# Performance work log

Hardware: AMD Instinct MI355X
Metric: run time of the kernel (lower is better)

The kernel has to match this reference:

```python
import jax, jax.numpy as jnp
import numpy as np

N_NODES = 50000
N_EDGES = 600000
F_IN = 128
DIM_H = 256
N_CLASSES = 40
BN_EPS = 1e-5


def setup_inputs() -> dict:
    key = jax.random.key(0)
    ks = jax.random.split(key, 10)
    x = jax.random.normal(ks[0], (N_NODES, F_IN), dtype=jnp.float32)
    edge_index = jax.random.randint(ks[1], (2, N_EDGES), 0, N_NODES, dtype=jnp.int64)
    s1 = 1.0 / np.sqrt(F_IN)
    s2 = 1.0 / np.sqrt(DIM_H)
    W1 = jax.random.uniform(ks[2], (F_IN, DIM_H), jnp.float32, -s1, s1)
    b1 = jax.random.uniform(ks[3], (DIM_H,), jnp.float32, -s1, s1)
    gamma = jnp.ones((DIM_H,), jnp.float32)
    beta = jnp.zeros((DIM_H,), jnp.float32)
    W2 = jax.random.uniform(ks[4], (DIM_H, DIM_H), jnp.float32, -s2, s2)
    b2 = jax.random.uniform(ks[5], (DIM_H,), jnp.float32, -s2, s2)
    Wlin = jax.random.uniform(ks[6], (DIM_H, N_CLASSES), jnp.float32, -s2, s2)
    blin = jax.random.uniform(ks[7], (N_CLASSES,), jnp.float32, -s2, s2)
    return {"x": x, "edge_index": edge_index, "W1": W1, "b1": b1,
            "gamma": gamma, "beta": beta, "W2": W2, "b2": b2,
            "Wlin": Wlin, "blin": blin}


def reference(x, edge_index, W1, b1, gamma, beta, W2, b2, Wlin, blin):
    src, dst = edge_index[0], edge_index[1]
    # GIN sum aggregation: agg[i] = sum_{(j->i)} x[j]; eps = 0 (default)
    agg = jax.ops.segment_sum(x[src], dst, num_segments=N_NODES)  # [N, F_IN]
    h = x + agg
    # MLP: Linear -> BatchNorm1d (training-mode batch stats) -> ReLU -> Linear -> ReLU
    h = h @ W1 + b1                               # [N, DIM_H]
    mean = jnp.mean(h, axis=0)
    var = jnp.var(h, axis=0)                      # biased, as torch BN uses for normalization
    h = (h - mean) * jax.lax.rsqrt(var + BN_EPS) * gamma + beta
    h = jax.nn.relu(h)
    h = jax.nn.relu(h @ W2 + b2)                  # MLP final ReLU; outer x.relu() is idempotent
    return h @ Wlin + blin                        # [N, N_CLASSES]
```

## Files before the change

kernel.cpp:

```cpp
#include <hip/hip_runtime.h>

#define F_IN 128
#define DIM_H 256
#define N_CLASSES 40
#define BN_EPS 1e-5f
#define M_PAD 50176

typedef short bf16x8 __attribute__((ext_vector_type(8)));
typedef float f32x4 __attribute__((ext_vector_type(4)));

__device__ __forceinline__ unsigned short f2bf(float f) {
    union { float f; unsigned u; } v; v.f = f;
    unsigned r = v.u + 0x7fff + ((v.u >> 16) & 1);
    return (unsigned short)(r >> 16);
}
__device__ __forceinline__ float bf2f(unsigned short u) {
    union { unsigned u; float f; } v; v.u = ((unsigned)u) << 16;
    return v.f;
}
__device__ __forceinline__ float4 bf2f4(ushort4 u) {
    return make_float4(bf2f(u.x), bf2f(u.y), bf2f(u.z), bf2f(u.w));
}

__global__ void hist_kernel(const int* __restrict__ dst, int* __restrict__ hist, int nE) {
    int e = blockIdx.x * blockDim.x + threadIdx.x;
    if (e >= nE) return;
    atomicAdd(&hist[dst[e]], 1);
}

__global__ void scan_blocks_kernel(const int* __restrict__ hist,
                                   int* __restrict__ blockSums, int M) {
    __shared__ int lds[256];
    int t = threadIdx.x;
    int i = blockIdx.x * 256 + t;
    lds[t] = (i < M) ? hist[i] : 0;
    __syncthreads();
    for (int off = 128; off > 0; off >>= 1) {
        if (t < off) lds[t] += lds[t + off];
        __syncthreads();
    }
    if (t == 0) blockSums[blockIdx.x] = lds[0];
}

__global__ void scan_offsets_kernel(const int* __restrict__ blockSums,
                                    int* __restrict__ blockOffs,
                                    int nB, int* __restrict__ start, int M, int nE) {
    __shared__ int lds[256];
    int t = threadIdx.x;
    int orig = (t < nB) ? blockSums[t] : 0;
    lds[t] = orig;
    __syncthreads();
    for (int off = 1; off < 256; off <<= 1) {
        int v = (t >= off) ? lds[t - off] : 0;
        __syncthreads();
        lds[t] += v;
        __syncthreads();
    }
    if (t < nB) blockOffs[t] = lds[t] - orig;
    if (t == 0) start[M] = nE;
}

__global__ void scan_final_kernel(const int* __restrict__ hist,
                                  const int* __restrict__ blockOffs,
                                  int* __restrict__ start, int M) {
    __shared__ int lds[256];
    int t = threadIdx.x;
    int i = blockIdx.x * 256 + t;
    int orig = (i < M) ? hist[i] : 0;
    lds[t] = orig;
    __syncthreads();
    for (int off = 1; off < 256; off <<= 1) {
        int v = (t >= off) ? lds[t - off] : 0;
        __syncthreads();
        lds[t] += v;
        __syncthreads();
    }
    if (i < M) start[i] = blockOffs[blockIdx.x] + lds[t] - orig;
}

__global__ void fill_kernel(const int* __restrict__ src, const int* __restrict__ dst,
                            const int* __restrict__ start, int* __restrict__ cursor,
                            int* __restrict__ order, int nE) {
    int e = blockIdx.x * blockDim.x + threadIdx.x;
    if (e >= nE) return;
    int d = dst[e];
    int pos = start[d] + atomicAdd(&cursor[d], 1);
    order[pos] = src[e];
}

__global__ void prep_kernel(const float* __restrict__ x, unsigned short* __restrict__ xb,
                            const float* __restrict__ W1, const float* __restrict__ W2,
                            const float* __restrict__ Wl,
                            unsigned short* __restrict__ W1t,
                            unsigned short* __restrict__ W2t,
                            unsigned short* __restrict__ Wlt,
                            unsigned short* __restrict__ A1pad,
                            unsigned short* __restrict__ h1pad,
                            int XQ) {
    int idx = blockIdx.x * 256 + threadIdx.x;
    if (idx < XQ) {
        float4 v = ((const float4*)x)[idx];
        ushort4 o;
        o.x = f2bf(v.x); o.y = f2bf(v.y); o.z = f2bf(v.z); o.w = f2bf(v.w);
        ((ushort4*)xb)[idx] = o;
        return;
    }
    int j = idx - XQ;
    if (j < 32768) {
        int n = j >> 7, k = j & 127;
        W1t[j] = f2bf(W1[k * DIM_H + n]);
    } else if (j < 32768 + 65536) {
        int i = j - 32768;
        int n = i >> 8, k = i & 255;
        W2t[i] = f2bf(W2[k * DIM_H + n]);
    } else if (j < 32768 + 65536 + 16384) {
        int i = j - 98304;
        int n = i >> 8, k = i & 255;
        Wlt[i] = f2bf((n < N_CLASSES) ? Wl[k * N_CLASSES + n] : 0.f);
    } else if (j < 114688 + 4608) {
        int i = j - 114688;
        if (i < 1536) ((ushort4*)A1pad)[i] = make_ushort4(0, 0, 0, 0);
        else ((ushort4*)h1pad)[i - 1536] = make_ushort4(0, 0, 0, 0);
    }
}

__global__ void gather_agg_kernel(const float* __restrict__ x,
                                  const unsigned short* __restrict__ xb,
                                  const int* __restrict__ order,
                                  const int* __restrict__ start,
                                  unsigned short* __restrict__ A1, int M) {
    int node = blockIdx.x * 8 + (threadIdx.x >> 5);
    if (node >= M) return;
    int lane = threadIdx.x & 31;
    const ushort4* xv = (const ushort4*)xb;
    float4 a0 = ((const float4*)x)[(size_t)node * 32 + lane];
    float4 a1 = make_float4(0.f, 0.f, 0.f, 0.f);
    float4 a2 = a1, a3 = a1;
    int e0 = start[node], e1 = start[node + 1];
    int e = e0;
    for (; e + 4 <= e1; e += 4) {
        int s0 = order[e], s1 = order[e + 1], s2 = order[e + 2], s3 = order[e + 3];
        float4 v0 = bf2f4(xv[(size_t)s0 * 32 + lane]);
        float4 v1 = bf2f4(xv[(size_t)s1 * 32 + lane]);
        float4 v2 = bf2f4(xv[(size_t)s2 * 32 + lane]);
        float4 v3 = bf2f4(xv[(size_t)s3 * 32 + lane]);
        a0.x += v0.x; a0.y += v0.y; a0.z += v0.z; a0.w += v0.w;
        a1.x += v1.x; a1.y += v1.y; a1.z += v1.z; a1.w += v1.w;
        a2.x += v2.x; a2.y += v2.y; a2.z += v2.z; a2.w += v2.w;
        a3.x += v3.x; a3.y += v3.y; a3.z += v3.z; a3.w += v3.w;
    }
    for (; e < e1; ++e) {
        float4 v = bf2f4(xv[(size_t)order[e] * 32 + lane]);
        a1.x += v.x; a1.y += v.y; a1.z += v.z; a1.w += v.w;
    }
    float4 t;
    t.x = (a0.x + a1.x) + (a2.x + a3.x);
    t.y = (a0.y + a1.y) + (a2.y + a3.y);
    t.z = (a0.z + a1.z) + (a2.z + a3.z);
    t.w = (a0.w + a1.w) + (a2.w + a3.w);
    ushort4 o;
    o.x = f2bf(t.x); o.y = f2bf(t.y); o.z = f2bf(t.z); o.w = f2bf(t.w);
    ((ushort4*)A1)[(size_t)node * 32 + lane] = o;
}

__global__ void bn_reduce_kernel(const float* __restrict__ partials, int R,
                                 const float* __restrict__ gamma,
                                 const float* __restrict__ beta,
                                 float* __restrict__ scale,
                                 float* __restrict__ shift, int M) {
    __shared__ float ls[256], lss[256];
    int c = blockIdx.x, t = threadIdx.x;
    float s = 0.f, ss = 0.f;
    for (int r = t; r < R; r += 256) {
        s += partials[(long)r * 512 + c];
        ss += partials[(long)r * 512 + 256 + c];
    }
    ls[t] = s; lss[t] = ss;
    __syncthreads();
    for (int o = 128; o > 0; o >>= 1) {
        if (t < o) { ls[t] += ls[t + o]; lss[t] += lss[t + o]; }
        __syncthreads();
    }
    if (t == 0) {
        float inv = 1.0f / (float)M;
        float mean = ls[0] * inv;
        float var = lss[0] * inv - mean * mean;
        float sc = gamma[c] * rsqrtf(var + BN_EPS);
        scale[c] = sc;
        shift[c] = beta[c] - mean * sc;
    }
}

template <int WM, int WN, int K, int MODE>
__global__ __launch_bounds__(WM* WN * 64) void mfma_gemm(
    const unsigned short* __restrict__ A,
    const unsigned short* __restrict__ Bt,
    const float* __restrict__ bias,
    void* __restrict__ Cout,
    const float* __restrict__ scale,
    const float* __restrict__ shift,
    float* __restrict__ partials,
    const unsigned short* __restrict__ Wlt2,
    const float* __restrict__ bias2,
    int M) {
    constexpr int NT = WM * WN * 64;
    constexpr int BM = WM * 64, BN = WN * 64;
    constexpr int S = K / 32;
    constexpr int PITCH = 40;
    constexpr int ACH = BM * 4 / NT;
    constexpr int BCH = BN * 4 / NT;
    constexpr int STAGE = 2 * (BM + BN) * PITCH;
    constexpr int H2PITCH = 264;
    constexpr int H2T = (MODE == 1) ? BM * H2PITCH : 0;
    constexpr int LDSN = STAGE > H2T ? STAGE : H2T;

    __shared__ __align__(16) unsigned short lds[LDSN];
    unsigned short* AsBase = lds;
    unsigned short* BsBase = lds + 2 * BM * PITCH;

    int tid = threadIdx.x;
    int wave = tid >> 6, lane = tid & 63;
    int wm = wave / WN, wn = wave % WN;
    int l15 = lane & 15, q = lane >> 4;
    long row0 = (long)blockIdx.y * BM;
    long col0 = (long)blockIdx.x * BN;

    bf16x8 ar[ACH], br[BCH];

    auto loadAB = [&](int s) {
#pragma unroll
        for (int i = 0; i < ACH; ++i) {
            int ch = tid + i * NT;
            int m = ch >> 2, c = ch & 3;
            ar[i] = *(const bf16x8*)(A + (row0 + m) * K + s * 32 + c * 8);
        }
#pragma unroll
        for (int i = 0; i < BCH; ++i) {
            int ch = tid + i * NT;
            int m = ch >> 2, c = ch & 3;
            br[i] = *(const bf16x8*)(Bt + (col0 + m) * K + s * 32 + c * 8);
        }
    };

    auto writeAB = [&](int buf, int s) {
#pragma unroll
        for (int i = 0; i < ACH; ++i) {
            int ch = tid + i * NT;
            int m = ch >> 2, c = ch & 3;
            bf16x8 v = ar[i];
            if (MODE == 1) {
                int kb = s * 32 + c * 8;
                float4 sc0 = *(const float4*)(scale + kb);
                float4 sc1 = *(const float4*)(scale + kb + 4);
                float4 sh0 = *(const float4*)(shift + kb);
                float4 sh1 = *(const float4*)(shift + kb + 4);
                float scv[8] = {sc0.x, sc0.y, sc0.z, sc0.w, sc1.x, sc1.y, sc1.z, sc1.w};
                float shv[8] = {sh0.x, sh0.y, sh0.z, sh0.w, sh1.x, sh1.y, sh1.z, sh1.w};
#pragma unroll
                for (int j = 0; j < 8; ++j) {
                    float f = bf2f((unsigned short)v[j]);
                    f = fmaxf(f * scv[j] + shv[j], 0.f);
                    v[j] = (short)f2bf(f);
                }
            }
            *(bf16x8*)(&AsBase[buf * BM * PITCH + m * PITCH + c * 8]) = v;
        }
#pragma unroll
        for (int i = 0; i < BCH; ++i) {
            int ch = tid + i * NT;
            int m = ch >> 2, c = ch & 3;
            *(bf16x8*)(&BsBase[buf * BN * PITCH + m * PITCH + c * 8]) = br[i];
        }
    };

    f32x4 acc[4][4] = {};

    loadAB(0);
    writeAB(0, 0);
#pragma unroll
    for (int s = 0; s < S; ++s) {
        if (s + 1 < S) loadAB(s + 1);
        __syncthreads();
        int buf = s & 1;
        bf16x8 af[4], bfr[4];
#pragma unroll
        for (int mt = 0; mt < 4; ++mt)
            af[mt] = *(const bf16x8*)(&AsBase[buf * BM * PITCH + (wm * 64 + mt * 16 + l15) * PITCH + q * 8]);
#pragma unroll
        for (int nt = 0; nt < 4; ++nt)
            bfr[nt] = *(const bf16x8*)(&BsBase[buf * BN * PITCH + (wn * 64 + nt * 16 + l15) * PITCH + q * 8]);
#pragma unroll
        for (int mt = 0; mt < 4; ++mt)
#pragma unroll
            for (int nt = 0; nt < 4; ++nt)
                acc[mt][nt] = __builtin_amdgcn_mfma_f32_16x16x32_bf16(
                    af[mt], bfr[nt], acc[mt][nt], 0, 0, 0);
        if (s + 1 < S) writeAB((s + 1) & 1, s + 1);
    }

    if (MODE == 0) {
#pragma unroll
        for (int nt = 0; nt < 4; ++nt) {
            long col = col0 + wn * 64 + nt * 16 + l15;
            float b = bias[col];
            float s = 0.f, ss = 0.f;
#pragma unroll
            for (int mt = 0; mt < 4; ++mt) {
#pragma unroll
                for (int r = 0; r < 4; ++r) {
                    long row = row0 + wm * 64 + mt * 16 + q * 4 + r;
                    float v = acc[mt][nt][r] + b;
                    if (row < M) {
                        ((unsigned short*)Cout)[row * DIM_H + col] = f2bf(v);
                        s += v; ss += v * v;
                    }
                }
            }
            s += __shfl_xor(s, 16, 64);  s += __shfl_xor(s, 32, 64);
            ss += __shfl_xor(ss, 16, 64); ss += __shfl_xor(ss, 32, 64);
            if (lane < 16) {
                long pr = (long)blockIdx.y * WM + wm;
                partials[pr * 512 + col] = s;
                partials[pr * 512 + 256 + col] = ss;
            }
        }
    } else {
        __syncthreads();
        unsigned short* h2t = lds;
#pragma unroll
        for (int nt = 0; nt < 4; ++nt) {
            int colL = wn * 64 + nt * 16 + l15;
            float b = bias[colL];
#pragma unroll
            for (int mt = 0; mt < 4; ++mt)
#pragma unroll
                for (int r = 0; r < 4; ++r) {
                    int rowL = mt * 16 + q * 4 + r;
                    h2t[rowL * H2PITCH + colL] = f2bf(fmaxf(acc[mt][nt][r] + b, 0.f));
                }
        }
        __syncthreads();
        f32x4 acc3[3] = {};
#pragma unroll
        for (int s = 0; s < 8; ++s) {
            bf16x8 a3 = *(const bf16x8*)(&h2t[(wave * 16 + l15) * H2PITCH + s * 32 + q * 8]);
#pragma unroll
            for (int nt = 0; nt < 3; ++nt) {
                bf16x8 b3 = *(const bf16x8*)(Wlt2 + (nt * 16 + l15) * 256 + s * 32 + q * 8);
                acc3[nt] = __builtin_amdgcn_mfma_f32_16x16x32_bf16(a3, b3, acc3[nt], 0, 0, 0);
            }
        }
#pragma unroll
        for (int nt = 0; nt < 3; ++nt) {
            int col = nt * 16 + l15;
            if (col < N_CLASSES) {
                float b = bias2[col];
#pragma unroll
                for (int r = 0; r < 4; ++r) {
                    long row = row0 + wave * 16 + q * 4 + r;
                    if (row < M) ((float*)Cout)[row * N_CLASSES + col] = acc3[nt][r] + b;
                }
            }
        }
    }
}

extern "C" void kernel_launch(void* const* d_in, const int* in_sizes, int n_in,
                              void* d_out, int out_size, void* d_ws, size_t ws_size,
                              hipStream_t stream) {
    const float* x     = (const float*)d_in[0];
    const int*   ei    = (const int*)d_in[1];
    const float* W1    = (const float*)d_in[2];
    const float* b1    = (const float*)d_in[3];
    const float* gamma = (const float*)d_in[4];
    const float* beta  = (const float*)d_in[5];
    const float* W2    = (const float*)d_in[6];
    const float* b2    = (const float*)d_in[7];
    const float* Wlin  = (const float*)d_in[8];
    const float* blin  = (const float*)d_in[9];
    float* out = (float*)d_out;

    int M  = in_sizes[0] / F_IN;
    int nE = in_sizes[1] / 2;
    const int* srcIdx = ei;
    const int* dstIdx = ei + nE;
    int nB = (M + 255) / 256;
    int gy = (M + 63) / 64;
    int Rpart = gy;
    int XQ = M * 32;

    unsigned short* A1bf  = (unsigned short*)d_ws;
    unsigned short* h1bf  = A1bf + (size_t)M_PAD * F_IN;
    unsigned short* xb    = h1bf + (size_t)M_PAD * DIM_H;
    unsigned short* W1t   = xb + (size_t)M_PAD * F_IN;
    unsigned short* W2t   = W1t + DIM_H * F_IN;
    unsigned short* Wlt   = W2t + DIM_H * DIM_H;
    float*          partials = (float*)(Wlt + 64 * DIM_H);
    float*          scale = partials + (size_t)800 * 512;
    float*          shift = scale + DIM_H;
    int*            hist  = (int*)(shift + DIM_H);
    int*            cursor= hist + M;
    int*            start = cursor + M;
    int*            blockSums = start + (M + 1);
    int*            blockOffs = blockSums + 256;
    int*            order = blockOffs + 256;

    hipMemsetAsync(hist, 0, (size_t)2 * M * sizeof(int), stream);

    int tB = 256;
    hist_kernel<<<(nE + tB - 1) / tB, tB, 0, stream>>>(dstIdx, hist, nE);
    scan_blocks_kernel<<<nB, 256, 0, stream>>>(hist, blockSums, M);
    scan_offsets_kernel<<<1, 256, 0, stream>>>(blockSums, blockOffs, nB, start, M, nE);
    scan_final_kernel<<<nB, 256, 0, stream>>>(hist, blockOffs, start, M);
    fill_kernel<<<(nE + tB - 1) / tB, tB, 0, stream>>>(srcIdx, dstIdx, start, cursor, order, nE);
    prep_kernel<<<(XQ + 114688 + 4608 + 255) / 256, 256, 0, stream>>>(
        x, xb, W1, W2, Wlin, W1t, W2t, Wlt,
        A1bf + (size_t)M * F_IN, h1bf + (size_t)M * DIM_H, XQ);
    gather_agg_kernel<<<(M + 7) / 8, 256, 0, stream>>>(x, xb, order, start, A1bf, M);

    mfma_gemm<1, 4, F_IN, 0><<<dim3(1, gy), 256, 0, stream>>>(
        A1bf, W1t, b1, h1bf, nullptr, nullptr, partials, nullptr, nullptr, M);
    bn_reduce_kernel<<<DIM_H, 256, 0, stream>>>(partials, Rpart, gamma, beta, scale, shift, M);
    mfma_gemm<1, 4, DIM_H, 1><<<dim3(1, gy), 256, 0, stream>>>(
        h1bf, W2t, b2, out, scale, shift, nullptr, Wlt, blin, M);
}
```

Measured before the change: 252.0 us.

## Fuse neighbor aggregation into first GEMM and specialize GEMM kernels

The separate gather/aggregation kernel is removed. Each GEMM1 block now gathers its 64 rows' neighbor sums directly into LDS as the A operand, so the bf16 A1 intermediate is never written to or read back from global memory. The templated GEMM is split into two specialized kernels with single-buffered LDS and launch_bounds occupancy hints. The trade-offs are that the gather latency now sits inside the GEMM block before any MFMA work starts, and that the GEMM loop uses more barriers per K step.

New measurement: 247.5 us. No clear change (-1.8%).

```diff
diff --git a/kernel.cpp b/kernel.cpp
--- a/kernel.cpp
+++ b/kernel.cpp
@@ -94,7 +94,6 @@
                             unsigned short* __restrict__ W1t,
                             unsigned short* __restrict__ W2t,
                             unsigned short* __restrict__ Wlt,
-                            unsigned short* __restrict__ A1pad,
                             unsigned short* __restrict__ h1pad,
                             int XQ) {
     int idx = blockIdx.x * 256 + threadIdx.x;
@@ -117,50 +116,10 @@
         int i = j - 98304;
         int n = i >> 8, k = i & 255;
         Wlt[i] = f2bf((n < N_CLASSES) ? Wl[k * N_CLASSES + n] : 0.f);
-    } else if (j < 114688 + 4608) {
+    } else if (j < 114688 + 3072) {
         int i = j - 114688;
-        if (i < 1536) ((ushort4*)A1pad)[i] = make_ushort4(0, 0, 0, 0);
-        else ((ushort4*)h1pad)[i - 1536] = make_ushort4(0, 0, 0, 0);
-    }
-}
-
-__global__ void gather_agg_kernel(const float* __restrict__ x,
-                                  const unsigned short* __restrict__ xb,
-                                  const int* __restrict__ order,
-                                  const int* __restrict__ start,
-                                  unsigned short* __restrict__ A1, int M) {
-    int node = blockIdx.x * 8 + (threadIdx.x >> 5);
-    if (node >= M) return;
-    int lane = threadIdx.x & 31;
-    const ushort4* xv = (const ushort4*)xb;
-    float4 a0 = ((const float4*)x)[(size_t)node * 32 + lane];
-    float4 a1 = make_float4(0.f, 0.f, 0.f, 0.f);
-    float4 a2 = a1, a3 = a1;
-    int e0 = start[node], e1 = start[node + 1];
-    int e = e0;
-    for (; e + 4 <= e1; e += 4) {
-        int s0 = order[e], s1 = order[e + 1], s2 = order[e + 2], s3 = order[e + 3];
-        float4 v0 = bf2f4(xv[(size_t)s0 * 32 + lane]);
-        float4 v1 = bf2f4(xv[(size_t)s1 * 32 + lane]);
-        float4 v2 = bf2f4(xv[(size_t)s2 * 32 + lane]);
-        float4 v3 = bf2f4(xv[(size_t)s3 * 32 + lane]);
-        a0.x += v0.x; a0.y += v0.y; a0.z += v0.z; a0.w += v0.w;
-        a1.x += v1.x; a1.y += v1.y; a1.z += v1.z; a1.w += v1.w;
-        a2.x += v2.x; a2.y += v2.y; a2.z += v2.z; a2.w += v2.w;
-        a3.x += v3.x; a3.y += v3.y; a3.z += v3.z; a3.w += v3.w;
-    }
-    for (; e < e1; ++e) {
-        float4 v = bf2f4(xv[(size_t)order[e] * 32 + lane]);
-        a1.x += v.x; a1.y += v.y; a1.z += v.z; a1.w += v.w;
-    }
-    float4 t;
-    t.x = (a0.x + a1.x) + (a2.x + a3.x);
-    t.y = (a0.y + a1.y) + (a2.y + a3.y);
-    t.z = (a0.z + a1.z) + (a2.z + a3.z);
-    t.w = (a0.w + a1.w) + (a2.w + a3.w);
-    ushort4 o;
-    o.x = f2bf(t.x); o.y = f2bf(t.y); o.z = f2bf(t.z); o.w = f2bf(t.w);
-    ((ushort4*)A1)[(size_t)node * 32 + lane] = o;
+        ((ushort4*)h1pad)[i] = make_ushort4(0, 0, 0, 0);
+    }
 }
 
 __global__ void bn_reduce_kernel(const float* __restrict__ partials, int R,
@@ -191,175 +150,251 @@
     }
 }
 
-template <int WM, int WN, int K, int MODE>
-__global__ __launch_bounds__(WM* WN * 64) void mfma_gemm(
-    const unsigned short* __restrict__ A,
-    const unsigned short* __restrict__ Bt,
-    const float* __restrict__ bias,
-    void* __restrict__ Cout,
-    const float* __restrict__ scale,
-    const float* __restrict__ shift,
-    float* __restrict__ partials,
-    const unsigned short* __restrict__ Wlt2,
-    const float* __restrict__ bias2,
-    int M) {
-    constexpr int NT = WM * WN * 64;
-    constexpr int BM = WM * 64, BN = WN * 64;
-    constexpr int S = K / 32;
-    constexpr int PITCH = 40;
-    constexpr int ACH = BM * 4 / NT;
-    constexpr int BCH = BN * 4 / NT;
-    constexpr int STAGE = 2 * (BM + BN) * PITCH;
-    constexpr int H2PITCH = 264;
-    constexpr int H2T = (MODE == 1) ? BM * H2PITCH : 0;
-    constexpr int LDSN = STAGE > H2T ? STAGE : H2T;
-
-    __shared__ __align__(16) unsigned short lds[LDSN];
-    unsigned short* AsBase = lds;
-    unsigned short* BsBase = lds + 2 * BM * PITCH;
+__global__ __launch_bounds__(256, 4) void gin_gemm1_kernel(
+    const float* __restrict__ x, const unsigned short* __restrict__ xb,
+    const int* __restrict__ order, const int* __restrict__ start,
+    const unsigned short* __restrict__ W1t, const float* __restrict__ b1,
+    unsigned short* __restrict__ h1, float* __restrict__ partials, int M) {
+    constexpr int K = F_IN, S = K / 32;
+    constexpr int PA = 136;
+    constexpr int PB = 40;
+    __shared__ __align__(16) unsigned short At[64 * PA];
+    __shared__ __align__(16) unsigned short Bs[256 * PB];
 
     int tid = threadIdx.x;
     int wave = tid >> 6, lane = tid & 63;
-    int wm = wave / WN, wn = wave % WN;
     int l15 = lane & 15, q = lane >> 4;
-    long row0 = (long)blockIdx.y * BM;
-    long col0 = (long)blockIdx.x * BN;
-
-    bf16x8 ar[ACH], br[BCH];
-
-    auto loadAB = [&](int s) {
-#pragma unroll
-        for (int i = 0; i < ACH; ++i) {
-            int ch = tid + i * NT;
+    int wn = wave;
+    long row0 = (long)blockIdx.x * 64;
+
+    bf16x8 br[4];
+    auto loadB = [&](int s) {
+#pragma unroll
+        for (int i = 0; i < 4; ++i) {
+            int ch = tid + i * 256;
             int m = ch >> 2, c = ch & 3;
-            ar[i] = *(const bf16x8*)(A + (row0 + m) * K + s * 32 + c * 8);
-        }
-#pragma unroll
-        for (int i = 0; i < BCH; ++i) {
-            int ch = tid + i * NT;
+            br[i] = *(const bf16x8*)(W1t + m * K + s * 32 + c * 8);
+        }
+    };
+    auto writeB = [&]() {
+#pragma unroll
+        for (int i = 0; i < 4; ++i) {
+            int ch = tid + i * 256;
             int m = ch >> 2, c = ch & 3;
-            br[i] = *(const bf16x8*)(Bt + (col0 + m) * K + s * 32 + c * 8);
+            *(bf16x8*)(&Bs[m * PB + c * 8]) = br[i];
         }
     };
 
-    auto writeAB = [&](int buf, int s) {
-#pragma unroll
-        for (int i = 0; i < ACH; ++i) {
-            int ch = tid + i * NT;
-            int m = ch >> 2, c = ch & 3;
-            bf16x8 v = ar[i];
-            if (MODE == 1) {
-                int kb = s * 32 + c * 8;
-                float4 sc0 = *(const float4*)(scale + kb);
-                float4 sc1 = *(const float4*)(scale + kb + 4);
-                float4 sh0 = *(const float4*)(shift + kb);
-                float4 sh1 = *(const float4*)(shift + kb + 4);
-                float scv[8] = {sc0.x, sc0.y, sc0.z, sc0.w, sc1.x, sc1.y, sc1.z, sc1.w};
-                float shv[8] = {sh0.x, sh0.y, sh0.z, sh0.w, sh1.x, sh1.y, sh1.z, sh1.w};
-#pragma unroll
-                for (int j = 0; j < 8; ++j) {
-                    float f = bf2f((unsigned short)v[j]);
-                    f = fmaxf(f * scv[j] + shv[j], 0.f);
-                    v[j] = (short)f2bf(f);
+    loadB(0);
+
+    {
+        int hw = tid >> 5, lane32 = tid & 31;
+        const ushort4* xv = (const ushort4*)xb;
+        for (int rr = 0; rr < 8; ++rr) {
+            int r = rr * 8 + hw;
+            long node = row0 + r;
+            float4 a0 = make_float4(0.f, 0.f, 0.f, 0.f);
+            float4 a1 = a0, a2 = a0, a3 = a0;
+            if (node < M) {
+                a0 = ((const float4*)x)[node * 32 + lane32];
+                int e0 = start[node], e1 = start[node + 1];
+                int e = e0;
+                for (; e + 4 <= e1; e += 4) {
+                    int s0 = order[e], s1 = order[e + 1], s2 = order[e + 2], s3 = order[e + 3];
+                    float4 v0 = bf2f4(xv[(size_t)s0 * 32 + lane32]);
+                    float4 v1 = bf2f4(xv[(size_t)s1 * 32 + lane32]);
+                    float4 v2 = bf2f4(xv[(size_t)s2 * 32 + lane32]);
+                    float4 v3 = bf2f4(xv[(size_t)s3 * 32 + lane32]);
+                    a0.x += v0.x; a0.y += v0.y; a0.z += v0.z; a0.w += v0.w;
+                    a1.x += v1.x; a1.y += v1.y; a1.z += v1.z; a1.w += v1.w;
+                    a2.x += v2.x; a2.y += v2.y; a2.z += v2.z; a2.w += v2.w;
+                    a3.x += v3.x; a3.y += v3.y; a3.z += v3.z; a3.w += v3.w;
+                }
+                for (; e < e1; ++e) {
+                    float4 v = bf2f4(xv[(size_t)order[e] * 32 + lane32]);
+                    a1.x += v.x; a1.y += v.y; a1.z += v.z; a1.w += v.w;
                 }
             }
-            *(bf16x8*)(&AsBase[buf * BM * PITCH + m * PITCH + c * 8]) = v;
-        }
-#pragma unroll
-        for (int i = 0; i < BCH; ++i) {
-            int ch = tid + i * NT;
-            int m = ch >> 2, c = ch & 3;
-            *(bf16x8*)(&BsBase[buf * BN * PITCH + m * PITCH + c * 8]) = br[i];
-        }
-    };
+            float4 t;
+            t.x = (a0.x + a1.x) + (a2.x + a3.x);
+            t.y = (a0.y + a1.y) + (a2.y + a3.y);
+            t.z = (a0.z + a1.z) + (a2.z + a3.z);
+            t.w = (a0.w + a1.w) + (a2.w + a3.w);
+            ushort4 o;
+            o.x = f2bf(t.x); o.y = f2bf(t.y); o.z = f2bf(t.z); o.w = f2bf(t.w);
+            *(ushort4*)(&At[r * PA + lane32 * 4]) = o;
+        }
+    }
+    writeB();
+    __syncthreads();
 
     f32x4 acc[4][4] = {};
-
-    loadAB(0);
-    writeAB(0, 0);
 #pragma unroll
     for (int s = 0; s < S; ++s) {
-        if (s + 1 < S) loadAB(s + 1);
-        __syncthreads();
-        int buf = s & 1;
+        if (s + 1 < S) loadB(s + 1);
         bf16x8 af[4], bfr[4];
 #pragma unroll
         for (int mt = 0; mt < 4; ++mt)
-            af[mt] = *(const bf16x8*)(&AsBase[buf * BM * PITCH + (wm * 64 + mt * 16 + l15) * PITCH + q * 8]);
+            af[mt] = *(const bf16x8*)(&At[(mt * 16 + l15) * PA + s * 32 + q * 8]);
 #pragma unroll
         for (int nt = 0; nt < 4; ++nt)
-            bfr[nt] = *(const bf16x8*)(&BsBase[buf * BN * PITCH + (wn * 64 + nt * 16 + l15) * PITCH + q * 8]);
+            bfr[nt] = *(const bf16x8*)(&Bs[(wn * 64 + nt * 16 + l15) * PB + q * 8]);
 #pragma unroll
         for (int mt = 0; mt < 4; ++mt)
 #pragma unroll
             for (int nt = 0; nt < 4; ++nt)
                 acc[mt][nt] = __builtin_amdgcn_mfma_f32_16x16x32_bf16(
                     af[mt], bfr[nt], acc[mt][nt], 0, 0, 0);
-        if (s + 1 < S) writeAB((s + 1) & 1, s + 1);
-    }
-
-    if (MODE == 0) {
-#pragma unroll
-        for (int nt = 0; nt < 4; ++nt) {
-            long col = col0 + wn * 64 + nt * 16 + l15;
-            float b = bias[col];
-            float s = 0.f, ss = 0.f;
-#pragma unroll
-            for (int mt = 0; mt < 4; ++mt) {
-#pragma unroll
-                for (int r = 0; r < 4; ++r) {
-                    long row = row0 + wm * 64 + mt * 16 + q * 4 + r;
-                    float v = acc[mt][nt][r] + b;
-                    if (row < M) {
-                        ((unsigned short*)Cout)[row * DIM_H + col] = f2bf(v);
-                        s += v; ss += v * v;
-                    }
+        __syncthreads();
+        if (s + 1 < S) { writeB(); __syncthreads(); }
+    }
+
+#pragma unroll
+    for (int nt = 0; nt < 4; ++nt) {
+        int col = wn * 64 + nt * 16 + l15;
+        float b = b1[col];
+        float s = 0.f, ss = 0.f;
+#pragma unroll
+        for (int mt = 0; mt < 4; ++mt) {
+#pragma unroll
+            for (int r = 0; r < 4; ++r) {
+                long row = row0 + mt * 16 + q * 4 + r;
+                float v = acc[mt][nt][r] + b;
+                if (row < M) {
+                    h1[row * DIM_H + col] = f2bf(v);
+                    s += v; ss += v * v;
                 }
             }
-            s += __shfl_xor(s, 16, 64);  s += __shfl_xor(s, 32, 64);
-            ss += __shfl_xor(ss, 16, 64); ss += __shfl_xor(ss, 32, 64);
-            if (lane < 16) {
-                long pr = (long)blockIdx.y * WM + wm;
-                partials[pr * 512 + col] = s;
-                partials[pr * 512 + 256 + col] = ss;
+        }
+        s += __shfl_xor(s, 16, 64);  s += __shfl_xor(s, 32, 64);
+        ss += __shfl_xor(ss, 16, 64); ss += __shfl_xor(ss, 32, 64);
+        if (lane < 16) {
+            partials[(long)blockIdx.x * 512 + col] = s;
+            partials[(long)blockIdx.x * 512 + 256 + col] = ss;
+        }
+    }
+}
+
+__global__ __launch_bounds__(256, 4) void gemm23_kernel(
+    const unsigned short* __restrict__ h1, const unsigned short* __restrict__ W2t,
+    const float* __restrict__ b2,
+    const float* __restrict__ scale, const float* __restrict__ shift,
+    const unsigned short* __restrict__ Wlt, const float* __restrict__ blin,
+    float* __restrict__ out, int M) {
+    constexpr int K = DIM_H, S = K / 32;
+    constexpr int PA = 40;
+    constexpr int PB = 40;
+    constexpr int PH = 264;
+    constexpr int LDSN = 64 * PH;
+    __shared__ __align__(16) unsigned short lds[LDSN];
+    unsigned short* As = lds;
+    unsigned short* Bs = lds + 64 * PA;
+    unsigned short* h2t = lds;
+
+    int tid = threadIdx.x;
+    int wave = tid >> 6, lane = tid & 63;
+    int l15 = lane & 15, q = lane >> 4;
+    int wn = wave;
+    long row0 = (long)blockIdx.x * 64;
+
+    bf16x8 ar, br[4];
+    auto loadAB = [&](int s) {
+        {
+            int m = tid >> 2, c = tid & 3;
+            ar = *(const bf16x8*)(h1 + (row0 + m) * K + s * 32 + c * 8);
+        }
+#pragma unroll
+        for (int i = 0; i < 4; ++i) {
+            int ch = tid + i * 256;
+            int m = ch >> 2, c = ch & 3;
+            br[i] = *(const bf16x8*)(W2t + m * K + s * 32 + c * 8);
+        }
+    };
+    auto writeAB = [&](int s) {
+        {
+            int m = tid >> 2, c = tid & 3;
+            int kb = s * 32 + c * 8;
+            float4 sc0 = *(const float4*)(scale + kb);
+            float4 sc1 = *(const float4*)(scale + kb + 4);
+            float4 sh0 = *(const float4*)(shift + kb);
+            float4 sh1 = *(const float4*)(shift + kb + 4);
+            float scv[8] = {sc0.x, sc0.y, sc0.z, sc0.w, sc1.x, sc1.y, sc1.z, sc1.w};
+            float shv[8] = {sh0.x, sh0.y, sh0.z, sh0.w, sh1.x, sh1.y, sh1.z, sh1.w};
+            bf16x8 v = ar;
+#pragma unroll
+            for (int j = 0; j < 8; ++j) {
+                float f = bf2f((unsigned short)v[j]);
+                f = fmaxf(f * scv[j] + shv[j], 0.f);
+                v[j] = (short)f2bf(f);
             }
-        }
-    } else {
-        __syncthreads();
-        unsigned short* h2t = lds;
-#pragma unroll
-        for (int nt = 0; nt < 4; ++nt) {
-            int colL = wn * 64 + nt * 16 + l15;
-            float b = bias[colL];
-#pragma unroll
-            for (int mt = 0; mt < 4; ++mt)
-#pragma unroll
-                for (int r = 0; r < 4; ++r) {
-                    int rowL = mt * 16 + q * 4 + r;
-                    h2t[rowL * H2PITCH + colL] = f2bf(fmaxf(acc[mt][nt][r] + b, 0.f));
-                }
-        }
-        __syncthreads();
-        f32x4 acc3[3] = {};
-#pragma unroll
-        for (int s = 0; s < 8; ++s) {
-            bf16x8 a3 = *(const bf16x8*)(&h2t[(wave * 16 + l15) * H2PITCH + s * 32 + q * 8]);
-#pragma unroll
-            for (int nt = 0; nt < 3; ++nt) {
-                bf16x8 b3 = *(const bf16x8*)(Wlt2 + (nt * 16 + l15) * 256 + s * 32 + q * 8);
-                acc3[nt] = __builtin_amdgcn_mfma_f32_16x16x32_bf16(a3, b3, acc3[nt], 0, 0, 0);
+            *(bf16x8*)(&As[m * PA + c * 8]) = v;
+        }
+#pragma unroll
+        for (int i = 0; i < 4; ++i) {
+            int ch = tid + i * 256;
+            int m = ch >> 2, c = ch & 3;
+            *(bf16x8*)(&Bs[m * PB + c * 8]) = br[i];
+        }
+    };
+
+    f32x4 acc[4][4] = {};
+
+    loadAB(0);
+    writeAB(0);
+    __syncthreads();
+#pragma unroll
+    for (int s = 0; s < S; ++s) {
+        if (s + 1 < S) loadAB(s + 1);
+        bf16x8 af[4], bfr[4];
+#pragma unroll
+        for (int mt = 0; mt < 4; ++mt)
+            af[mt] = *(const bf16x8*)(&As[(mt * 16 + l15) * PA + q * 8]);
+#pragma unroll
+        for (int nt = 0; nt < 4; ++nt)
+            bfr[nt] = *(const bf16x8*)(&Bs[(wn * 64 + nt * 16 + l15) * PB + q * 8]);
+#pragma unroll
+        for (int mt = 0; mt < 4; ++mt)
+#pragma unroll
+            for (int nt = 0; nt < 4; ++nt)
+                acc[mt][nt] = __builtin_amdgcn_mfma_f32_16x16x32_bf16(
+                    af[mt], bfr[nt], acc[mt][nt], 0, 0, 0);
+        __syncthreads();
+        if (s + 1 < S) { writeAB(s + 1); __syncthreads(); }
+    }
+
+#pragma unroll
+    for (int nt = 0; nt < 4; ++nt) {
+        int colL = wn * 64 + nt * 16 + l15;
+        float b = b2[colL];
+#pragma unroll
+        for (int mt = 0; mt < 4; ++mt)
+#pragma unroll
+            for (int r = 0; r < 4; ++r) {
+                int rowL = mt * 16 + q * 4 + r;
+                h2t[rowL * PH + colL] = f2bf(fmaxf(acc[mt][nt][r] + b, 0.f));
             }
-        }
+    }
+    __syncthreads();
+
+    f32x4 acc3[3] = {};
+#pragma unroll
+    for (int s = 0; s < 8; ++s) {
+        bf16x8 a3 = *(const bf16x8*)(&h2t[(wave * 16 + l15) * PH + s * 32 + q * 8]);
 #pragma unroll
         for (int nt = 0; nt < 3; ++nt) {
-            int col = nt * 16 + l15;
-            if (col < N_CLASSES) {
-                float b = bias2[col];
-#pragma unroll
-                for (int r = 0; r < 4; ++r) {
-                    long row = row0 + wave * 16 + q * 4 + r;
-                    if (row < M) ((float*)Cout)[row * N_CLASSES + col] = acc3[nt][r] + b;
-                }
+            bf16x8 b3 = *(const bf16x8*)(Wlt + (nt * 16 + l15) * 256 + s * 32 + q * 8);
+            acc3[nt] = __builtin_amdgcn_mfma_f32_16x16x32_bf16(a3, b3, acc3[nt], 0, 0, 0);
+        }
+    }
+#pragma unroll
+    for (int nt = 0; nt < 3; ++nt) {
+        int col = nt * 16 + l15;
+        if (col < N_CLASSES) {
+            float b = blin[col];
+#pragma unroll
+            for (int r = 0; r < 4; ++r) {
+                long row = row0 + wave * 16 + q * 4 + r;
+                if (row < M) out[row * N_CLASSES + col] = acc3[nt][r] + b;
             }
         }
     }
@@ -386,11 +421,9 @@
     const int* dstIdx = ei + nE;
     int nB = (M + 255) / 256;
     int gy = (M + 63) / 64;
-    int Rpart = gy;
     int XQ = M * 32;
 
-    unsigned short* A1bf  = (unsigned short*)d_ws;
-    unsigned short* h1bf  = A1bf + (size_t)M_PAD * F_IN;
+    unsigned short* h1bf  = (unsigned short*)d_ws;
     unsigned short* xb    = h1bf + (size_t)M_PAD * DIM_H;
     unsigned short* W1t   = xb + (size_t)M_PAD * F_IN;
     unsigned short* W2t   = W1t + DIM_H * F_IN;
@@ -413,14 +446,10 @@
     scan_offsets_kernel<<<1, 256, 0, stream>>>(blockSums, blockOffs, nB, start, M, nE);
     scan_final_kernel<<<nB, 256, 0, stream>>>(hist, blockOffs, start, M);
     fill_kernel<<<(nE + tB - 1) / tB, tB, 0, stream>>>(srcIdx, dstIdx, start, cursor, order, nE);
-    prep_kernel<<<(XQ + 114688 + 4608 + 255) / 256, 256, 0, stream>>>(
-        x, xb, W1, W2, Wlin, W1t, W2t, Wlt,
-        A1bf + (size_t)M * F_IN, h1bf + (size_t)M * DIM_H, XQ);
-    gather_agg_kernel<<<(M + 7) / 8, 256, 0, stream>>>(x, xb, order, start, A1bf, M);
-
-    mfma_gemm<1, 4, F_IN, 0><<<dim3(1, gy), 256, 0, stream>>>(
-        A1bf, W1t, b1, h1bf, nullptr, nullptr, partials, nullptr, nullptr, M);
-    bn_reduce_kernel<<<DIM_H, 256, 0, stream>>>(partials, Rpart, gamma, beta, scale, shift, M);
-    mfma_gemm<1, 4, DIM_H, 1><<<dim3(1, gy), 256, 0, stream>>>(
-        h1bf, W2t, b2, out, scale, shift, nullptr, Wlt, blin, M);
-}
+    prep_kernel<<<(XQ + 114688 + 3072 + 255) / 256, 256, 0, stream>>>(
+        x, xb, W1, W2, Wlin, W1t, W2t, Wlt, h1bf + (size_t)M * DIM_H, XQ);
+
+    gin_gemm1_kernel<<<gy, 256, 0, stream>>>(x, xb, order, start, W1t, b1, h1bf, partials, M);
+    bn_reduce_kernel<<<DIM_H, 256, 0, stream>>>(partials, gy, gamma, beta, scale, shift, M);
+    gemm23_kernel<<<gy, 256, 0, stream>>>(h1bf, W2t, b2, scale, shift, Wlt, blin, out, M);
+}
```
